# Kernel tuning notes

Measured on AMD Instinct MI355X. Metric: run time of the kernel, lower is better.

Reference implementation:

```python
import jax, jax.numpy as jnp
import numpy as np

H, D = 8, 64          # num_heads, head_dim
DM = 512              # model/feature dim for q,k,v,pos
B, N, M = 8, 1024, 1024


def relative_shift(x):
    # x: [B, H, N, M] -> Transformer-XL pad/reshape shift trick
    b, h, n, m = x.shape
    x = jnp.pad(x, ((0, 0), (0, 0), (0, 0), (1, 0)))      # [B,H,N,M+1]
    x = x.reshape(b, h, m + 1, n)
    x = x[:, :, 1:, :].reshape(b, h, n, m)
    return x


def setup_inputs() -> dict:
    key = jax.random.key(0)
    ks = jax.random.split(key, 11)
    s = 0.05  # small init scale for numerical stability (glorot-ish)
    return {
        "query": jax.random.normal(ks[0], (B, N, DM), jnp.float32),
        "key": jax.random.normal(ks[1], (B, M, DM), jnp.float32),
        "value": jax.random.normal(ks[2], (B, M, DM), jnp.float32),
        "pos": jax.random.normal(ks[3], (B, M, DM), jnp.float32),
        "query_kernel": jax.random.normal(ks[4], (H, DM, D), jnp.float32) * s,
        "key_kernel": jax.random.normal(ks[5], (H, DM, D), jnp.float32) * s,
        "value_kernel": jax.random.normal(ks[6], (H, DM, D), jnp.float32) * s,
        "pos_kernel": jax.random.normal(ks[7], (H, DM, D), jnp.float32) * s,
        "projection_kernel": jax.random.normal(ks[8], (H, D, DM), jnp.float32) * s,
        "pos_bias_u": jax.random.normal(ks[9], (H, D), jnp.float32) * s,
        "pos_bias_v": jax.random.normal(ks[10], (H, D), jnp.float32) * s,
    }


def reference(query, key, value, pos, query_kernel, key_kernel, value_kernel,
              pos_kernel, projection_kernel, pos_bias_u, pos_bias_v):
    # per-head projections
    q = jnp.einsum("bni,hid->bnhd", query, query_kernel)
    k = jnp.einsum("bmi,hid->bmhd", key, key_kernel)
    v = jnp.einsum("bmi,hid->bmhd", value, value_kernel)
    p = jnp.einsum("bmi,hid->bmhd", pos, pos_kernel)

    q_u = q + pos_bias_u  # broadcast [H,D] over [B,N,H,D]
    q_v = q + pos_bias_v

    logits_u = jnp.einsum("bnhd,bmhd->bhnm", q_u, k)
    logits_v = relative_shift(jnp.einsum("bnhd,bmhd->bhnm", q_v, p))

    m = logits_u.shape[3]
    logits = (logits_u + logits_v[:, :, :, :m]) / jnp.sqrt(
        jnp.asarray(D, logits_u.dtype))

    attn = jax.nn.softmax(logits, axis=-1)            # [B,H,N,M]
    ctx = jnp.einsum("bhnm,bmhd->bnhd", attn, v)      # [B,N,H,D]
    out = jnp.einsum("bnhd,hdo->bno", ctx, projection_kernel)
    return out
```

## Files before the change

kernel.cpp:

```cpp
#include <hip/hip_runtime.h>
#include <hip/hip_bf16.h>
#include <math.h>

#define SB 8
#define SS 1024
#define SDM 512
#define SH 8
#define SD 64

typedef unsigned short ushort;
typedef __attribute__((ext_vector_type(8))) short bf16x8;
typedef __attribute__((ext_vector_type(4))) float f32x4;

#define MFMA16(a, b, c) __builtin_amdgcn_mfma_f32_16x16x32_bf16(a, b, c, 0, 0, 0)

static __device__ __forceinline__ ushort f2b(float f) {
    union { float f; unsigned u; } v; v.f = f;
    unsigned r = v.u + 0x7FFF + ((v.u >> 16) & 1);
    return (ushort)(r >> 16);
}

static __device__ __forceinline__ void gll16(const void* g, void* l) {
    __builtin_amdgcn_global_load_lds(
        (const __attribute__((address_space(1))) unsigned int*)g,
        (__attribute__((address_space(3))) unsigned int*)l, 16, 0, 0);
}

__global__ __launch_bounds__(256) void convert_x_kernel(
    const float* __restrict__ q, const float* __restrict__ k,
    const float* __restrict__ v, const float* __restrict__ p,
    ushort* __restrict__ xbf)
{
    const int which = blockIdx.y;
    const float* src = (which == 0) ? q : (which == 1) ? k : (which == 2) ? v : p;
    ushort* dst = xbf + (size_t)which * ((size_t)SB * SS * SDM);
    size_t i = ((size_t)blockIdx.x * 256 + threadIdx.x) * 8;
    float4 a = *(const float4*)(src + i);
    float4 b = *(const float4*)(src + i + 4);
    union { ushort u[8]; uint4 v4; } o;
    o.u[0] = f2b(a.x); o.u[1] = f2b(a.y); o.u[2] = f2b(a.z); o.u[3] = f2b(a.w);
    o.u[4] = f2b(b.x); o.u[5] = f2b(b.y); o.u[6] = f2b(b.z); o.u[7] = f2b(b.w);
    *(uint4*)(dst + i) = o.v4;
}

__global__ __launch_bounds__(256) void convert_w_kernel(
    const float* __restrict__ qw, const float* __restrict__ kw,
    const float* __restrict__ vw, const float* __restrict__ pw,
    const float* __restrict__ projw, ushort* __restrict__ wt)
{
    const int which = blockIdx.y;
    const int idx = blockIdx.x * 256 + threadIdx.x;
    const int c  = idx >> 9;
    const int kk = idx & 511;
    float val;
    if (which < 4) {
        const float* W = (which == 0) ? qw : (which == 1) ? kw : (which == 2) ? vw : pw;
        const int h = c >> 6, d = c & 63;
        val = W[(size_t)h * SDM * SD + (size_t)kk * SD + d];
    } else {
        val = projw[(size_t)kk * SDM + c];
    }
    wt[(size_t)which * SDM * SDM + (size_t)c * SDM + kk] = f2b(val);
}

__global__ __launch_bounds__(256) void projmm_kernel(
    const ushort* __restrict__ xbf, const ushort* __restrict__ wt,
    const float* __restrict__ bias_u, const float* __restrict__ bias_v,
    ushort* __restrict__ quo, ushort* __restrict__ qvo,
    ushort* __restrict__ ko, ushort* __restrict__ po,
    ushort* __restrict__ vto)
{
    __shared__ ushort Asm[128 * 32];
    __shared__ ushort Bsm[128 * 32];

    const int tid  = threadIdx.x;
    const int wave = tid >> 6, lane = tid & 63;
    const int quad = lane >> 4, l15 = lane & 15;
    const int which = blockIdx.z;
    const int row0 = blockIdx.x * 128;
    const int col0 = blockIdx.y * 128;
    const int wr = wave >> 1, wc = wave & 1;

    const ushort* A  = xbf + (size_t)which * ((size_t)SB * SS * SDM) + (size_t)row0 * SDM;
    const ushort* Bw = wt  + (size_t)which * (SDM * SDM) + (size_t)col0 * SDM;

    f32x4 acc[4][4];
#pragma unroll
    for (int i = 0; i < 4; ++i)
#pragma unroll
        for (int j = 0; j < 4; ++j) acc[i][j] = (f32x4){0.f, 0.f, 0.f, 0.f};

    for (int k0 = 0; k0 < SDM; k0 += 32) {
#pragma unroll
        for (int j = 0; j < 2; ++j) {
            int t = j * 256 + tid;
            int r = t >> 2, kp = (t & 3) * 8;
            gll16(A  + (size_t)r * SDM + k0 + kp, (char*)Asm + t * 16);
            gll16(Bw + (size_t)r * SDM + k0 + kp, (char*)Bsm + t * 16);
        }
        __syncthreads();

        bf16x8 af[4], bfr[4];
#pragma unroll
        for (int mt = 0; mt < 4; ++mt)
            af[mt] = *(const bf16x8*)&Asm[(wr * 64 + mt * 16 + l15) * 32 + quad * 8];
#pragma unroll
        for (int nt = 0; nt < 4; ++nt)
            bfr[nt] = *(const bf16x8*)&Bsm[(wc * 64 + nt * 16 + l15) * 32 + quad * 8];
#pragma unroll
        for (int mt = 0; mt < 4; ++mt)
#pragma unroll
            for (int nt = 0; nt < 4; ++nt)
                acc[mt][nt] = MFMA16(af[mt], bfr[nt], acc[mt][nt]);
        __syncthreads();
    }

    const float SC = 0.125f;
#pragma unroll
    for (int nt = 0; nt < 4; ++nt) {
        const int C = col0 + wc * 64 + nt * 16 + l15;
        const int h = C >> 6, d = C & 63;
        if (which == 0) {
            const float bu = bias_u[C];
            const float bv = bias_v[C];
#pragma unroll
            for (int mt = 0; mt < 4; ++mt) {
                const int Rb = row0 + wr * 64 + mt * 16 + quad * 4;
                const int b = Rb >> 10;
                const int n = Rb & 1023;
                const size_t base = ((size_t)(b * SH + h) * SS + n) * SD + d;
#pragma unroll
                for (int r = 0; r < 4; ++r) {
                    quo[base + (size_t)r * SD] = f2b((acc[mt][nt][r] + bu) * SC);
                    qvo[base + (size_t)r * SD] = f2b((acc[mt][nt][r] + bv) * SC);
                }
            }
        } else if (which == 1 || which == 3) {
            ushort* out = (which == 1) ? ko : po;
#pragma unroll
            for (int mt = 0; mt < 4; ++mt) {
                const int Rb = row0 + wr * 64 + mt * 16 + quad * 4;
                const int b = Rb >> 10;
                const int n = Rb & 1023;
                const size_t base = ((size_t)(b * SH + h) * SS + n) * SD + d;
#pragma unroll
                for (int r = 0; r < 4; ++r)
                    out[base + (size_t)r * SD] = f2b(acc[mt][nt][r]);
            }
        } else {
#pragma unroll
            for (int mt = 0; mt < 4; ++mt) {
                const int Rb = row0 + wr * 64 + mt * 16 + quad * 4;
                const int b = Rb >> 10;
                const int n = Rb & 1023;
                union { ushort u[4]; uint2 v2; } pk;
#pragma unroll
                for (int r = 0; r < 4; ++r) pk.u[r] = f2b(acc[mt][nt][r]);
                const size_t base = (size_t)(b * SH + h) * SS * SD
                                  + ((size_t)((n >> 6) * 64 + d)) * 64 + (n & 63);
                *(uint2*)&vto[base] = pk.v2;
            }
        }
    }
}

static __device__ __forceinline__ bf16x8 sfrag(const ushort* buf, int row, int seg) {
    return *(const bf16x8*)&buf[(size_t)row * 64 + ((seg ^ (row & 7)) * 8)];
}

__global__ __launch_bounds__(256) void attn_kernel(
    const ushort* __restrict__ qu, const ushort* __restrict__ qv,
    const ushort* __restrict__ kk, const ushort* __restrict__ pp,
    const ushort* __restrict__ vt, ushort* __restrict__ ctx)
{
    __shared__ ushort Kb[64 * 64];
    __shared__ ushort Pb[128 * 64];
    __shared__ float  Glds[4][16][80];
    __shared__ ushort Plds[4][16][72];

    const int tid  = threadIdx.x;
    const int wave = tid >> 6;
    const int lane = tid & 63;
    const int quad = lane >> 4;
    const int l15  = lane & 15;

    const int id   = blockIdx.x;
    const int xcd  = id & 7;
    const int slot = id >> 3;
    const int bhid = xcd * 8 + (slot >> 4);
    const int nt   = slot & 15;
    const int b    = bhid >> 3;
    const int h    = bhid & 7;
    const int n0   = nt * 64;

    const size_t bh   = (size_t)(b * SH + h);
    const ushort* qu_bh = qu + bh * SS * SD;
    const ushort* qv_bh = qv + bh * SS * SD;
    const ushort* k_bh  = kk + bh * SS * SD;
    const ushort* p_bh  = pp + bh * SS * SD;
    const ushort* vt_bh = vt + bh * SS * SD;

    const int mcD = n0 >> 6;

    const int arow  = n0 + wave * 16 + l15;
    const int arow2 = (arow + 1 < SS) ? arow + 1 : SS - 1;

    bf16x8 a_u0  = *(const bf16x8*)(qu_bh + (size_t)arow  * SD + quad * 8);
    bf16x8 a_u1  = *(const bf16x8*)(qu_bh + (size_t)arow  * SD + quad * 8 + 32);
    bf16x8 a_vl0 = *(const bf16x8*)(qv_bh + (size_t)arow  * SD + quad * 8);
    bf16x8 a_vl1 = *(const bf16x8*)(qv_bh + (size_t)arow  * SD + quad * 8 + 32);
    bf16x8 a_vu0 = *(const bf16x8*)(qv_bh + (size_t)arow2 * SD + quad * 8);
    bf16x8 a_vu1 = *(const bf16x8*)(qv_bh + (size_t)arow2 * SD + quad * 8 + 32);

    float lsum[4] = {0.f, 0.f, 0.f, 0.f};
    f32x4 O[4];
#pragma unroll
    for (int dt = 0; dt < 4; ++dt) O[dt] = (f32x4){0.f, 0.f, 0.f, 0.f};

    float  (*Gl)[80] = Glds[wave];
    ushort (*Pl)[72] = Plds[wave];

    auto stage = [&](int mc) {
        const int m0s = mc * 64;
        const int cb  = (mc <= mcD) ? (m0s - n0 + 960) : (m0s - n0 - 65);
#pragma unroll
        for (int it = 0; it < 2; ++it) {
            int t = it * 256 + tid;
            int r = t >> 3, s = t & 7;
            gll16(k_bh + (size_t)(m0s + r) * 64 + ((s ^ (r & 7)) * 8),
                  (char*)Kb + t * 16);
        }
#pragma unroll
        for (int it = 0; it < 4; ++it) {
            int t = it * 256 + tid;
            int r = t >> 3, s = t & 7;
            int c = cb + r; c = (c < 0) ? 0 : (c > SS - 1 ? SS - 1 : c);
            gll16(p_bh + (size_t)c * 64 + ((s ^ (r & 7)) * 8),
                  (char*)Pb + t * 16);
        }
    };

    stage(0);

    for (int mc = 0; mc < 16; ++mc) {
        const int m0 = mc * 64;
        const int diff = m0 - n0;
        const bool lowerband = (mc <= mcD);

        __syncthreads();

        f32x4 S[4];
#pragma unroll
        for (int mt = 0; mt < 4; ++mt) {
            const int r = mt * 16 + l15;
            f32x4 c = (f32x4){0.f, 0.f, 0.f, 0.f};
            c = MFMA16(a_u0, sfrag(Kb, r, quad), c);
            c = MFMA16(a_u1, sfrag(Kb, r, quad + 4), c);
            S[mt] = c;
        }

        float sv[4][4];
#pragma unroll
        for (int mt = 0; mt < 4; ++mt)
#pragma unroll
            for (int r = 0; r < 4; ++r) sv[mt][r] = 0.f;

        {
            const bf16x8 av0 = lowerband ? a_vl0 : a_vu0;
            const bf16x8 av1 = lowerband ? a_vl1 : a_vu1;
#pragma unroll
            for (int ti = 0; ti < 5; ++ti) {
                const int t = (3 - wave + ti) * 16 + l15;
                f32x4 g = (f32x4){0.f, 0.f, 0.f, 0.f};
                g = MFMA16(av0, sfrag(Pb, t, quad), g);
                g = MFMA16(av1, sfrag(Pb, t, quad + 4), g);
#pragma unroll
                for (int r = 0; r < 4; ++r)
                    Gl[quad * 4 + r][ti * 16 + l15] = g[r];
            }
#pragma unroll
            for (int mt = 0; mt < 4; ++mt) {
                const int mloc = mt * 16 + l15;
#pragma unroll
                for (int r = 0; r < 4; ++r) {
                    const int q4r = quad * 4 + r;
                    const int d1 = diff + mloc - (wave * 16 + q4r);
                    const bool use = lowerband ? (d1 <= 0) : (d1 >= 2);
                    if (use) sv[mt][r] = Gl[q4r][mloc - q4r + 15];
                }
            }
        }

        if (mc == mcD) {
            const int cbase = diff - 65;
            bf16x8 pu0[5], pu1[5];
#pragma unroll
            for (int ti = 0; ti < 5; ++ti) {
                int t = (3 - wave + ti) * 16 + l15;
                int c = cbase + t;
                c = (c < 0) ? 0 : (c > SS - 1 ? SS - 1 : c);
                const ushort* pr = p_bh + (size_t)c * SD + quad * 8;
                pu0[ti] = *(const bf16x8*)pr;
                pu1[ti] = *(const bf16x8*)(pr + 32);
            }
#pragma unroll
            for (int ti = 0; ti < 5; ++ti) {
                f32x4 g = (f32x4){0.f, 0.f, 0.f, 0.f};
                g = MFMA16(a_vu0, pu0[ti], g);
                g = MFMA16(a_vu1, pu1[ti], g);
#pragma unroll
                for (int r = 0; r < 4; ++r)
                    Gl[quad * 4 + r][ti * 16 + l15] = g[r];
            }
#pragma unroll
            for (int mt = 0; mt < 4; ++mt) {
                const int mloc = mt * 16 + l15;
#pragma unroll
                for (int r = 0; r < 4; ++r) {
                    const int q4r = quad * 4 + r;
                    const int d1 = diff + mloc - (wave * 16 + q4r);
                    if (d1 >= 2) sv[mt][r] = Gl[q4r][mloc - q4r + 15];
                }
            }
        }

        __syncthreads();
        if (mc + 1 < 16) stage(mc + 1);

        bf16x8 vb0[4], vb1[4];
#pragma unroll
        for (int dt = 0; dt < 4; ++dt) {
            const ushort* vp = vt_bh + (size_t)(m0 + dt * 16 + l15) * 64 + quad * 8;
            vb0[dt] = *(const bf16x8*)vp;
            vb1[dt] = *(const bf16x8*)(vp + 32);
        }

        float e[4][4];
#pragma unroll
        for (int mt = 0; mt < 4; ++mt)
#pragma unroll
            for (int r = 0; r < 4; ++r) {
                e[mt][r] = __expf(S[mt][r] + sv[mt][r]);
                lsum[r] += e[mt][r];
            }

#pragma unroll
        for (int mt = 0; mt < 4; ++mt)
#pragma unroll
            for (int r = 0; r < 4; ++r)
                Pl[quad * 4 + r][mt * 16 + l15] = f2b(e[mt][r]);

        bf16x8 ap0 = *(const bf16x8*)&Pl[l15][quad * 8];
        bf16x8 ap1 = *(const bf16x8*)&Pl[l15][32 + quad * 8];
#pragma unroll
        for (int dt = 0; dt < 4; ++dt) {
            O[dt] = MFMA16(ap0, vb0[dt], O[dt]);
            O[dt] = MFMA16(ap1, vb1[dt], O[dt]);
        }
    }

#pragma unroll
    for (int mask = 1; mask <= 8; mask <<= 1)
#pragma unroll
        for (int r = 0; r < 4; ++r)
            lsum[r] += __shfl_xor(lsum[r], mask, 16);

    float inv[4];
#pragma unroll
    for (int r = 0; r < 4; ++r) inv[r] = 1.f / lsum[r];

#pragma unroll
    for (int dt = 0; dt < 4; ++dt)
#pragma unroll
        for (int r = 0; r < 4; ++r) {
            int nn = n0 + wave * 16 + quad * 4 + r;
            ctx[((size_t)b * SS + nn) * (SH * SD) + h * SD + dt * 16 + l15] =
                f2b(O[dt][r] * inv[r]);
        }
}

__global__ __launch_bounds__(256) void outproj_kernel(
    const ushort* __restrict__ ctx, const ushort* __restrict__ wt,
    float* __restrict__ out)
{
    __shared__ ushort Asm[128 * 32];
    __shared__ ushort Bsm[128 * 32];

    const int tid  = threadIdx.x;
    const int wave = tid >> 6, lane = tid & 63;
    const int quad = lane >> 4, l15 = lane & 15;
    const int row0 = blockIdx.x * 128;
    const int col0 = blockIdx.y * 128;
    const int wr = wave >> 1, wc = wave & 1;

    const ushort* A  = ctx + (size_t)row0 * SDM;
    const ushort* Bw = wt + (size_t)4 * (SDM * SDM) + (size_t)col0 * SDM;

    f32x4 acc[4][4];
#pragma unroll
    for (int i = 0; i < 4; ++i)
#pragma unroll
        for (int j = 0; j < 4; ++j) acc[i][j] = (f32x4){0.f, 0.f, 0.f, 0.f};

    for (int k0 = 0; k0 < SDM; k0 += 32) {
#pragma unroll
        for (int j = 0; j < 2; ++j) {
            int t = j * 256 + tid;
            int r = t >> 2, kp = (t & 3) * 8;
            gll16(A  + (size_t)r * SDM + k0 + kp, (char*)Asm + t * 16);
            gll16(Bw + (size_t)r * SDM + k0 + kp, (char*)Bsm + t * 16);
        }
        __syncthreads();

        bf16x8 af[4], bfr[4];
#pragma unroll
        for (int mt = 0; mt < 4; ++mt)
            af[mt] = *(const bf16x8*)&Asm[(wr * 64 + mt * 16 + l15) * 32 + quad * 8];
#pragma unroll
        for (int nt = 0; nt < 4; ++nt)
            bfr[nt] = *(const bf16x8*)&Bsm[(wc * 64 + nt * 16 + l15) * 32 + quad * 8];
#pragma unroll
        for (int mt = 0; mt < 4; ++mt)
#pragma unroll
            for (int nt = 0; nt < 4; ++nt)
                acc[mt][nt] = MFMA16(af[mt], bfr[nt], acc[mt][nt]);
        __syncthreads();
    }

#pragma unroll
    for (int mt = 0; mt < 4; ++mt)
#pragma unroll
        for (int nt = 0; nt < 4; ++nt) {
            const int R = row0 + wr * 64 + mt * 16 + quad * 4;
            const int C = col0 + wc * 64 + nt * 16 + l15;
#pragma unroll
            for (int r = 0; r < 4; ++r)
                out[(size_t)(R + r) * SDM + C] = acc[mt][nt][r];
        }
}

extern "C" void kernel_launch(void* const* d_in, const int* in_sizes, int n_in,
                              void* d_out, int out_size, void* d_ws, size_t ws_size,
                              hipStream_t stream)
{
    const float* query  = (const float*)d_in[0];
    const float* key    = (const float*)d_in[1];
    const float* value  = (const float*)d_in[2];
    const float* pos    = (const float*)d_in[3];
    const float* qw     = (const float*)d_in[4];
    const float* kw     = (const float*)d_in[5];
    const float* vw     = (const float*)d_in[6];
    const float* pw     = (const float*)d_in[7];
    const float* projw  = (const float*)d_in[8];
    const float* bias_u = (const float*)d_in[9];
    const float* bias_v = (const float*)d_in[10];

    char* w = (char*)d_ws;
    const size_t MB = 1024 * 1024;
    ushort* xbf = (ushort*)w;
    ushort* quo = (ushort*)(w + 32 * MB);
    ushort* qvo = (ushort*)(w + 40 * MB);
    ushort* ko  = (ushort*)(w + 48 * MB);
    ushort* po  = (ushort*)(w + 56 * MB);
    ushort* vto = (ushort*)(w + 64 * MB);
    ushort* wt  = (ushort*)(w + 72 * MB);
    ushort* ctx = (ushort*)w;

    dim3 gcx(2048, 4);
    convert_x_kernel<<<gcx, 256, 0, stream>>>(query, key, value, pos, xbf);
    dim3 gcw(1024, 5);
    convert_w_kernel<<<gcw, 256, 0, stream>>>(qw, kw, vw, pw, projw, wt);

    dim3 g1(64, 4, 4);
    projmm_kernel<<<g1, 256, 0, stream>>>(xbf, wt, bias_u, bias_v,
                                          quo, qvo, ko, po, vto);

    attn_kernel<<<dim3(1024), 256, 0, stream>>>(quo, qvo, ko, po, vto, ctx);

    dim3 g3(64, 4);
    outproj_kernel<<<g3, 256, 0, stream>>>(ctx, wt, (float*)d_out);
}
```

Before: 270.9 us.

## Merge convert kernels, stage projection epilogue via LDS, double-buffer attention K/P tiles

Fuses the input and weight bf16 conversion kernels into one launch and has each weight-conversion thread pack eight values into a single vector store. The projection GEMM epilogue now writes its tile to shared memory and then issues coalesced 16-byte row stores, including for the transposed V layout, instead of scattered 2-byte stores. The attention kernel double-buffers the K and P LDS tiles so the next chunk's async load is issued right after the barrier, hoists the V fragment loads earlier, and reuses the G scratch buffer for P to save LDS. The extra LDS (a 34KB staging tile, doubled K/P buffers) may reduce occupancy.

```diff
diff --git a/kernel.cpp b/kernel.cpp
--- a/kernel.cpp
+++ b/kernel.cpp
@@ -26,41 +26,49 @@
         (__attribute__((address_space(3))) unsigned int*)l, 16, 0, 0);
 }
 
-__global__ __launch_bounds__(256) void convert_x_kernel(
+#define XTHREADS 2097152
+#define WTHREADS 163840
+__global__ __launch_bounds__(256) void convert_kernel(
     const float* __restrict__ q, const float* __restrict__ k,
     const float* __restrict__ v, const float* __restrict__ p,
-    ushort* __restrict__ xbf)
-{
-    const int which = blockIdx.y;
-    const float* src = (which == 0) ? q : (which == 1) ? k : (which == 2) ? v : p;
-    ushort* dst = xbf + (size_t)which * ((size_t)SB * SS * SDM);
-    size_t i = ((size_t)blockIdx.x * 256 + threadIdx.x) * 8;
-    float4 a = *(const float4*)(src + i);
-    float4 b = *(const float4*)(src + i + 4);
-    union { ushort u[8]; uint4 v4; } o;
-    o.u[0] = f2b(a.x); o.u[1] = f2b(a.y); o.u[2] = f2b(a.z); o.u[3] = f2b(a.w);
-    o.u[4] = f2b(b.x); o.u[5] = f2b(b.y); o.u[6] = f2b(b.z); o.u[7] = f2b(b.w);
-    *(uint4*)(dst + i) = o.v4;
-}
-
-__global__ __launch_bounds__(256) void convert_w_kernel(
     const float* __restrict__ qw, const float* __restrict__ kw,
     const float* __restrict__ vw, const float* __restrict__ pw,
-    const float* __restrict__ projw, ushort* __restrict__ wt)
+    const float* __restrict__ projw,
+    ushort* __restrict__ xbf, ushort* __restrict__ wt)
 {
-    const int which = blockIdx.y;
-    const int idx = blockIdx.x * 256 + threadIdx.x;
-    const int c  = idx >> 9;
-    const int kk = idx & 511;
-    float val;
-    if (which < 4) {
-        const float* W = (which == 0) ? qw : (which == 1) ? kw : (which == 2) ? vw : pw;
-        const int h = c >> 6, d = c & 63;
-        val = W[(size_t)h * SDM * SD + (size_t)kk * SD + d];
+    const int gid = blockIdx.x * 256 + threadIdx.x;
+    if (gid < XTHREADS) {
+        const int which = gid >> 19;
+        const float* src = (which == 0) ? q : (which == 1) ? k : (which == 2) ? v : p;
+        ushort* dst = xbf + (size_t)which * ((size_t)SB * SS * SDM);
+        size_t i = (size_t)(gid & 524287) * 8;
+        float4 a = *(const float4*)(src + i);
+        float4 b = *(const float4*)(src + i + 4);
+        union { ushort u[8]; uint4 v4; } o;
+        o.u[0] = f2b(a.x); o.u[1] = f2b(a.y); o.u[2] = f2b(a.z); o.u[3] = f2b(a.w);
+        o.u[4] = f2b(b.x); o.u[5] = f2b(b.y); o.u[6] = f2b(b.z); o.u[7] = f2b(b.w);
+        *(uint4*)(dst + i) = o.v4;
     } else {
-        val = projw[(size_t)kk * SDM + c];
+        const int wid = gid - XTHREADS;
+        const int which = wid >> 15;
+        const int local = wid & 32767;
+        const int c  = local >> 6;
+        const int k0 = (local & 63) * 8;
+        union { ushort u[8]; uint4 v4; } o;
+        if (which < 4) {
+            const float* W = (which == 0) ? qw : (which == 1) ? kw
+                           : (which == 2) ? vw : pw;
+            const int h = c >> 6, d = c & 63;
+            const float* base = W + (size_t)h * SDM * SD + (size_t)k0 * SD + d;
+#pragma unroll
+            for (int j = 0; j < 8; ++j) o.u[j] = f2b(base[(size_t)j * SD]);
+        } else {
+            const float* base = projw + (size_t)k0 * SDM + c;
+#pragma unroll
+            for (int j = 0; j < 8; ++j) o.u[j] = f2b(base[(size_t)j * SDM]);
+        }
+        *(uint4*)&wt[(size_t)which * SDM * SDM + (size_t)c * SDM + k0] = o.v4;
     }
-    wt[(size_t)which * SDM * SDM + (size_t)c * SDM + kk] = f2b(val);
 }
 
 __global__ __launch_bounds__(256) void projmm_kernel(
@@ -72,6 +80,7 @@
 {
     __shared__ ushort Asm[128 * 32];
     __shared__ ushort Bsm[128 * 32];
+    __shared__ ushort Ct[128][136];
 
     const int tid  = threadIdx.x;
     const int wave = tid >> 6, lane = tid & 63;
@@ -116,50 +125,98 @@
     }
 
     const float SC = 0.125f;
-#pragma unroll
-    for (int nt = 0; nt < 4; ++nt) {
-        const int C = col0 + wc * 64 + nt * 16 + l15;
-        const int h = C >> 6, d = C & 63;
-        if (which == 0) {
-            const float bu = bias_u[C];
-            const float bv = bias_v[C];
+
+    const int strow = tid >> 1;
+    const int sthalf = tid & 1;
+
+    if (which == 0) {
+#pragma unroll
+        for (int nt = 0; nt < 4; ++nt) {
+            const int lc = wc * 64 + nt * 16 + l15;
+            const float bu = bias_u[col0 + lc];
 #pragma unroll
             for (int mt = 0; mt < 4; ++mt) {
-                const int Rb = row0 + wr * 64 + mt * 16 + quad * 4;
-                const int b = Rb >> 10;
-                const int n = Rb & 1023;
-                const size_t base = ((size_t)(b * SH + h) * SS + n) * SD + d;
-#pragma unroll
-                for (int r = 0; r < 4; ++r) {
-                    quo[base + (size_t)r * SD] = f2b((acc[mt][nt][r] + bu) * SC);
-                    qvo[base + (size_t)r * SD] = f2b((acc[mt][nt][r] + bv) * SC);
-                }
-            }
-        } else if (which == 1 || which == 3) {
+                const int lr = wr * 64 + mt * 16 + quad * 4;
+#pragma unroll
+                for (int r = 0; r < 4; ++r)
+                    Ct[lr + r][lc] = f2b((acc[mt][nt][r] + bu) * SC);
+            }
+        }
+        __syncthreads();
+        {
+            const int R = row0 + strow, b = R >> 10, n = R & 1023;
+            const int C = col0 + sthalf * 64, h = C >> 6;
+            uint4* dst = (uint4*)(quo + ((size_t)(b * SH + h) * SS + n) * SD);
+            const uint4* src = (const uint4*)&Ct[strow][sthalf * 64];
+#pragma unroll
+            for (int j = 0; j < 8; ++j) dst[j] = src[j];
+        }
+        __syncthreads();
+#pragma unroll
+        for (int nt = 0; nt < 4; ++nt) {
+            const int lc = wc * 64 + nt * 16 + l15;
+            const float bv = bias_v[col0 + lc];
+#pragma unroll
+            for (int mt = 0; mt < 4; ++mt) {
+                const int lr = wr * 64 + mt * 16 + quad * 4;
+#pragma unroll
+                for (int r = 0; r < 4; ++r)
+                    Ct[lr + r][lc] = f2b((acc[mt][nt][r] + bv) * SC);
+            }
+        }
+        __syncthreads();
+        {
+            const int R = row0 + strow, b = R >> 10, n = R & 1023;
+            const int C = col0 + sthalf * 64, h = C >> 6;
+            uint4* dst = (uint4*)(qvo + ((size_t)(b * SH + h) * SS + n) * SD);
+            const uint4* src = (const uint4*)&Ct[strow][sthalf * 64];
+#pragma unroll
+            for (int j = 0; j < 8; ++j) dst[j] = src[j];
+        }
+    } else if (which == 1 || which == 3) {
+#pragma unroll
+        for (int nt = 0; nt < 4; ++nt) {
+            const int lc = wc * 64 + nt * 16 + l15;
+#pragma unroll
+            for (int mt = 0; mt < 4; ++mt) {
+                const int lr = wr * 64 + mt * 16 + quad * 4;
+#pragma unroll
+                for (int r = 0; r < 4; ++r)
+                    Ct[lr + r][lc] = f2b(acc[mt][nt][r]);
+            }
+        }
+        __syncthreads();
+        {
             ushort* out = (which == 1) ? ko : po;
+            const int R = row0 + strow, b = R >> 10, n = R & 1023;
+            const int C = col0 + sthalf * 64, h = C >> 6;
+            uint4* dst = (uint4*)(out + ((size_t)(b * SH + h) * SS + n) * SD);
+            const uint4* src = (const uint4*)&Ct[strow][sthalf * 64];
+#pragma unroll
+            for (int j = 0; j < 8; ++j) dst[j] = src[j];
+        }
+    } else {
+#pragma unroll
+        for (int nt = 0; nt < 4; ++nt) {
+            const int lc = wc * 64 + nt * 16 + l15;
 #pragma unroll
             for (int mt = 0; mt < 4; ++mt) {
-                const int Rb = row0 + wr * 64 + mt * 16 + quad * 4;
-                const int b = Rb >> 10;
-                const int n = Rb & 1023;
-                const size_t base = ((size_t)(b * SH + h) * SS + n) * SD + d;
+                const int lr = wr * 64 + mt * 16 + quad * 4;
 #pragma unroll
                 for (int r = 0; r < 4; ++r)
-                    out[base + (size_t)r * SD] = f2b(acc[mt][nt][r]);
-            }
-        } else {
-#pragma unroll
-            for (int mt = 0; mt < 4; ++mt) {
-                const int Rb = row0 + wr * 64 + mt * 16 + quad * 4;
-                const int b = Rb >> 10;
-                const int n = Rb & 1023;
-                union { ushort u[4]; uint2 v2; } pk;
-#pragma unroll
-                for (int r = 0; r < 4; ++r) pk.u[r] = f2b(acc[mt][nt][r]);
-                const size_t base = (size_t)(b * SH + h) * SS * SD
-                                  + ((size_t)((n >> 6) * 64 + d)) * 64 + (n & 63);
-                *(uint2*)&vto[base] = pk.v2;
-            }
+                    Ct[lc][lr + r] = f2b(acc[mt][nt][r]);
+            }
+        }
+        __syncthreads();
+        {
+            const int C = col0 + strow, h = C >> 6, d = C & 63;
+            const int b = row0 >> 10;
+            const int nloc = (row0 & 1023) + sthalf * 64;
+            uint4* dst = (uint4*)(vto + (size_t)(b * SH + h) * SS * SD
+                                  + ((size_t)((nloc >> 6) * 64 + d)) * 64);
+            const uint4* src = (const uint4*)&Ct[strow][sthalf * 64];
+#pragma unroll
+            for (int j = 0; j < 8; ++j) dst[j] = src[j];
         }
     }
 }
@@ -173,10 +230,9 @@
     const ushort* __restrict__ kk, const ushort* __restrict__ pp,
     const ushort* __restrict__ vt, ushort* __restrict__ ctx)
 {
-    __shared__ ushort Kb[64 * 64];
-    __shared__ ushort Pb[128 * 64];
+    __shared__ ushort KbBuf[2][64 * 64];
+    __shared__ ushort PbBuf[2][128 * 64];
     __shared__ float  Glds[4][16][80];
-    __shared__ ushort Plds[4][16][72];
 
     const int tid  = threadIdx.x;
     const int wave = tid >> 6;
@@ -218,44 +274,57 @@
     for (int dt = 0; dt < 4; ++dt) O[dt] = (f32x4){0.f, 0.f, 0.f, 0.f};
 
     float  (*Gl)[80] = Glds[wave];
-    ushort (*Pl)[72] = Plds[wave];
-
-    auto stage = [&](int mc) {
+    ushort (*Pl)[72] = (ushort (*)[72])Glds[wave];
+
+    auto stage = [&](int mc, int buf) {
         const int m0s = mc * 64;
         const int cb  = (mc <= mcD) ? (m0s - n0 + 960) : (m0s - n0 - 65);
+        char* Kd = (char*)KbBuf[buf];
+        char* Pd = (char*)PbBuf[buf];
 #pragma unroll
         for (int it = 0; it < 2; ++it) {
             int t = it * 256 + tid;
             int r = t >> 3, s = t & 7;
-            gll16(k_bh + (size_t)(m0s + r) * 64 + ((s ^ (r & 7)) * 8),
-                  (char*)Kb + t * 16);
+            gll16(k_bh + (size_t)(m0s + r) * 64 + ((s ^ (r & 7)) * 8), Kd + t * 16);
         }
 #pragma unroll
         for (int it = 0; it < 4; ++it) {
             int t = it * 256 + tid;
             int r = t >> 3, s = t & 7;
             int c = cb + r; c = (c < 0) ? 0 : (c > SS - 1 ? SS - 1 : c);
-            gll16(p_bh + (size_t)c * 64 + ((s ^ (r & 7)) * 8),
-                  (char*)Pb + t * 16);
+            gll16(p_bh + (size_t)c * 64 + ((s ^ (r & 7)) * 8), Pd + t * 16);
         }
     };
 
-    stage(0);
+    stage(0, 0);
 
     for (int mc = 0; mc < 16; ++mc) {
         const int m0 = mc * 64;
         const int diff = m0 - n0;
         const bool lowerband = (mc <= mcD);
-
-        __syncthreads();
+        const int cur = mc & 1;
+
+        __syncthreads();
+        if (mc + 1 < 16) stage(mc + 1, cur ^ 1);
+
+        const ushort* Kc = KbBuf[cur];
+        const ushort* Pc = PbBuf[cur];
+
+        bf16x8 vb0[4], vb1[4];
+#pragma unroll
+        for (int dt = 0; dt < 4; ++dt) {
+            const ushort* vp = vt_bh + (size_t)(m0 + dt * 16 + l15) * 64 + quad * 8;
+            vb0[dt] = *(const bf16x8*)vp;
+            vb1[dt] = *(const bf16x8*)(vp + 32);
+        }
 
         f32x4 S[4];
 #pragma unroll
         for (int mt = 0; mt < 4; ++mt) {
             const int r = mt * 16 + l15;
             f32x4 c = (f32x4){0.f, 0.f, 0.f, 0.f};
-            c = MFMA16(a_u0, sfrag(Kb, r, quad), c);
-            c = MFMA16(a_u1, sfrag(Kb, r, quad + 4), c);
+            c = MFMA16(a_u0, sfrag(Kc, r, quad), c);
+            c = MFMA16(a_u1, sfrag(Kc, r, quad + 4), c);
             S[mt] = c;
         }
 
@@ -272,8 +341,8 @@
             for (int ti = 0; ti < 5; ++ti) {
                 const int t = (3 - wave + ti) * 16 + l15;
                 f32x4 g = (f32x4){0.f, 0.f, 0.f, 0.f};
-                g = MFMA16(av0, sfrag(Pb, t, quad), g);
-                g = MFMA16(av1, sfrag(Pb, t, quad + 4), g);
+                g = MFMA16(av0, sfrag(Pc, t, quad), g);
+                g = MFMA16(av1, sfrag(Pc, t, quad + 4), g);
 #pragma unroll
                 for (int r = 0; r < 4; ++r)
                     Gl[quad * 4 + r][ti * 16 + l15] = g[r];
@@ -322,17 +391,6 @@
                     if (d1 >= 2) sv[mt][r] = Gl[q4r][mloc - q4r + 15];
                 }
             }
-        }
-
-        __syncthreads();
-        if (mc + 1 < 16) stage(mc + 1);
-
-        bf16x8 vb0[4], vb1[4];
-#pragma unroll
-        for (int dt = 0; dt < 4; ++dt) {
-            const ushort* vp = vt_bh + (size_t)(m0 + dt * 16 + l15) * 64 + quad * 8;
-            vb0[dt] = *(const bf16x8*)vp;
-            vb1[dt] = *(const bf16x8*)(vp + 32);
         }
 
         float e[4][4];
@@ -466,10 +524,8 @@
     ushort* wt  = (ushort*)(w + 72 * MB);
     ushort* ctx = (ushort*)w;
 
-    dim3 gcx(2048, 4);
-    convert_x_kernel<<<gcx, 256, 0, stream>>>(query, key, value, pos, xbf);
-    dim3 gcw(1024, 5);
-    convert_w_kernel<<<gcw, 256, 0, stream>>>(qw, kw, vw, pw, projw, wt);
+    convert_kernel<<<dim3(8832), 256, 0, stream>>>(
+        query, key, value, pos, qw, kw, vw, pw, projw, xbf, wt);
 
     dim3 g1(64, 4, 4);
     projmm_kernel<<<g1, 256, 0, stream>>>(xbf, wt, bias_u, bias_v,
```

New measurement: 279.1 us. 1.03x slower.
